# Kernel optimization log

Measured on AMD Instinct MI355X. Metric: run time of the kernel, lower is better.

Reference implementation:

```python
import jax, jax.numpy as jnp
import numpy as np
from jax import lax

HEADS, DIM_HEAD = 4, 64
INNER = HEADS * DIM_HEAD              # 256
FEAT_DIM = MAP_DIM = OUT_DIM = 128
EXPANDED = 4 * OUT_DIM                # 512 (MBConv expansion)
MAP_SIZE = (8, 8, 8)
EPS = 1e-5


def conv3d(x, w, groups=1):
    # x: NCDHW, w: OIDHW ([out, in/groups, kd, kh, kw]); stride 1, 'same' padding
    return lax.conv_general_dilated(x, w, (1, 1, 1), 'SAME',
                                    feature_group_count=groups,
                                    dimension_numbers=('NCDHW', 'OIDHW', 'NCDHW'))


def inorm(x):
    # InstanceNorm3d (affine=False): normalize over spatial dims per sample/channel
    m = x.mean((2, 3, 4), keepdims=True)
    v = ((x - m) ** 2).mean((2, 3, 4), keepdims=True)
    return (x - m) * lax.rsqrt(v + EPS)


def _split_heads(t, spatial):
    # 'b (dim_head heads) d h w -> b heads (d h w) dim_head'
    B = t.shape[0]
    N = spatial[0] * spatial[1] * spatial[2]
    return t.reshape(B, DIM_HEAD, HEADS, N).transpose(0, 2, 3, 1)


def _merge_heads(t, spatial):
    # 'b heads n dim_head -> b (dim_head heads) d h w'
    B = t.shape[0]
    return t.transpose(0, 3, 1, 2).reshape(B, DIM_HEAD * HEADS, *spatial)


def setup_inputs() -> dict:
    key = jax.random.key(0)
    ks = jax.random.split(key, 16)
    r = lambda k, s: jax.random.normal(k, s, jnp.float32) * 0.05
    return {
        'x': jax.random.normal(ks[0], (2, FEAT_DIM, 24, 24, 24), jnp.float32),
        'semantic_map': jax.random.normal(ks[1], (2, MAP_DIM) + MAP_SIZE, jnp.float32),
        'w_fqv_dw': r(ks[2], (FEAT_DIM, 1, 3, 3, 3)),
        'w_fqv_pw': r(ks[3], (2 * INNER, FEAT_DIM, 1, 1, 1)),
        'w_mqv':    r(ks[4], (2 * INNER, MAP_DIM, 1, 1, 1)),
        'w_fout_dw': r(ks[5], (INNER, 1, 3, 3, 3)),
        'w_fout_pw': r(ks[6], (OUT_DIM, INNER, 1, 1, 1)),
        'w_mout':   r(ks[7], (MAP_DIM, INNER, 1, 1, 1)),
        'w_exp':    r(ks[8], (EXPANDED, OUT_DIM, 1, 1, 1)),
        'w_dw':     r(ks[9], (EXPANDED, 1, 3, 3, 3)),
        'w_se1':    r(ks[10], (EXPANDED // 4, EXPANDED, 1, 1, 1)),
        'b_se1':    jnp.zeros((EXPANDED // 4,), jnp.float32),
        'w_se2':    r(ks[11], (EXPANDED, EXPANDED // 4, 1, 1, 1)),
        'b_se2':    jnp.zeros((EXPANDED,), jnp.float32),
        'w_pw':     r(ks[12], (OUT_DIM, EXPANDED, 1, 1, 1)),
    }


def _mbconv(x, w_exp, w_dw, w_se1, b_se1, w_se2, b_se2, w_pw):
    # MBConv (preact ConvNormAct blocks, InstanceNorm + ReLU, SE, identity shortcut)
    h = conv3d(jax.nn.relu(inorm(x)), w_exp)
    h = conv3d(jax.nn.relu(inorm(h)), w_dw, groups=EXPANDED)
    s = h.mean((2, 3, 4), keepdims=True)                       # squeeze
    s = jax.nn.relu(conv3d(s, w_se1) + b_se1[None, :, None, None, None])
    s = jax.nn.sigmoid(conv3d(s, w_se2) + b_se2[None, :, None, None, None])
    h = h * s
    h = conv3d(inorm(h), w_pw)                                 # pointwise, act=False
    return h + x


def reference(x, semantic_map, w_fqv_dw, w_fqv_pw, w_mqv, w_fout_dw, w_fout_pw,
              w_mout, w_exp, w_dw, w_se1, b_se1, w_se2, b_se2, w_pw):
    B, C, D, H, W = x.shape
    feat = inorm(x)
    m = inorm(semantic_map)

    # QV projections: depthwise-separable for feat, 1x1 for map
    fqv = conv3d(conv3d(feat, w_fqv_dw, groups=FEAT_DIM), w_fqv_pw)
    fq, fv = jnp.split(fqv, 2, axis=1)
    mqv = conv3d(m, w_mqv)
    mq, mv = jnp.split(mqv, 2, axis=1)

    fq = _split_heads(fq, (D, H, W))   # [B, h, Nf, dh]
    fv = _split_heads(fv, (D, H, W))
    mq = _split_heads(mq, MAP_SIZE)    # [B, h, Nm, dh]
    mv = _split_heads(mv, MAP_SIZE)

    # shared score matrix, dual-direction softmax
    attn = jnp.einsum('bhid,bhjd->bhij', fq, mq) * (DIM_HEAD ** -0.5)
    feat_map_attn = jax.nn.softmax(attn, axis=-1)   # over map tokens j
    map_feat_attn = jax.nn.softmax(attn, axis=-2)   # over feat tokens i

    feat_out = jnp.einsum('bhij,bhjd->bhid', feat_map_attn, mv)   # [B,h,Nf,dh]
    map_out = jnp.einsum('bhji,bhjd->bhid', map_feat_attn, fv)    # [B,h,Nm,dh]

    feat_out = _merge_heads(feat_out, (D, H, W))
    map_out = _merge_heads(map_out, MAP_SIZE)

    feat_out = conv3d(conv3d(feat_out, w_fout_dw, groups=INNER), w_fout_pw)
    map_out = conv3d(map_out, w_mout)

    out = feat_out + x   # shortcut is identity (feat_dim == out_dim)
    out = _mbconv(out, w_exp, w_dw, w_se1, b_se1, w_se2, b_se2, w_pw)
    map_out = map_out + semantic_map
    return out, map_out
```

## Files before the change

### kernel.cpp

```cpp
#include <hip/hip_runtime.h>
#include <hip/hip_bf16.h>
#include <cstddef>

#define NF 13824
#define NM 512
#define NIC 27

typedef __attribute__((ext_vector_type(8))) short bf16x8;
typedef __attribute__((ext_vector_type(4))) float f32x4;

__device__ __forceinline__ void gload16(const float* g, float* l){
  __builtin_amdgcn_global_load_lds((const __attribute__((address_space(1))) void*)g,
                                   (__attribute__((address_space(3))) void*)l, 16, 0, 0);
}

__global__ void k_transpose6(const float* __restrict__ s0, float* __restrict__ d0,
                             const float* __restrict__ s1, float* __restrict__ d1,
                             const float* __restrict__ s2, float* __restrict__ d2,
                             const float* __restrict__ s3, float* __restrict__ d3,
                             const float* __restrict__ s4, float* __restrict__ d4,
                             const float* __restrict__ s5, float* __restrict__ d5){
  const float* W; float* WT; int Cout, Cin;
  switch (blockIdx.y){
    case 0: W=s0; WT=d0; Cout=512; Cin=128; break;
    case 1: W=s1; WT=d1; Cout=512; Cin=128; break;
    case 2: W=s2; WT=d2; Cout=128; Cin=256; break;
    case 3: W=s3; WT=d3; Cout=128; Cin=256; break;
    case 4: W=s4; WT=d4; Cout=512; Cin=128; break;
    default: W=s5; WT=d5; Cout=128; Cin=512; break;
  }
  int idx = blockIdx.x*256 + threadIdx.x;
  if (idx >= Cout*Cin) return;
  int co = idx / Cin, ci = idx % Cin;
  WT[(size_t)ci*Cout + co] = W[idx];
}

__global__ void k_stats(const float* __restrict__ in, float2* __restrict__ st, int N,
                        float2* __restrict__ tf){
  int row = blockIdx.x;
  const float* p = in + (size_t)row*N;
  float s=0.f, q=0.f;
  int n4 = N/4;
  for (int i=threadIdx.x; i<n4; i+=256){
    float4 v = *(const float4*)(p + i*4);
    s += v.x+v.y+v.z+v.w;
    q += v.x*v.x+v.y*v.y+v.z*v.z+v.w*v.w;
  }
  __shared__ float rs[256], rq[256];
  rs[threadIdx.x]=s; rq[threadIdx.x]=q;
  __syncthreads();
  for (int o=128;o>0;o>>=1){
    if (threadIdx.x<o){ rs[threadIdx.x]+=rs[threadIdx.x+o]; rq[threadIdx.x]+=rq[threadIdx.x+o]; }
    __syncthreads();
  }
  if (threadIdx.x==0){
    float m = rs[0]/N;
    float v = rq[0]/N - m*m;
    if (v<0.f) v=0.f;
    st[row] = make_float2(m, v);
    if (tf){
      float a = rsqrtf(v + 1e-5f);
      tf[row] = make_float2(a, -m*a);
    }
  }
}

__global__ void k_make_tf(const float2* __restrict__ st, const float* __restrict__ sbuf,
                          float2* __restrict__ tf, int rows){
  int i = blockIdx.x*256 + threadIdx.x;
  if (i>=rows) return;
  float s = sbuf ? sbuf[i] : 1.f;
  float2 mv = st[i];
  float a = s*rsqrtf(s*s*mv.y + 1e-5f);
  tf[i] = make_float2(a, -mv.x*a);
}

__global__ void k_red(const float2* __restrict__ part, int nparts, int rows,
                      float invN, float2* __restrict__ tf){
  int w = threadIdx.x>>6, l = threadIdx.x&63;
  int row = blockIdx.x*4 + w;
  if (row >= rows) return;
  const float2* p = part + (size_t)row*nparts;
  float s=0.f, q=0.f;
  for (int k=l; k<nparts; k+=64){ float2 v = p[k]; s += v.x; q += v.y; }
  s += __shfl_xor(s,1); s += __shfl_xor(s,2); s += __shfl_xor(s,4);
  s += __shfl_xor(s,8); s += __shfl_xor(s,16); s += __shfl_xor(s,32);
  q += __shfl_xor(q,1); q += __shfl_xor(q,2); q += __shfl_xor(q,4);
  q += __shfl_xor(q,8); q += __shfl_xor(q,16); q += __shfl_xor(q,32);
  if (l==0){
    float m = s*invN;
    float v = q*invN - m*m;
    if (v<0.f) v=0.f;
    float a = rsqrtf(v + 1e-5f);
    tf[row] = make_float2(a, -m*a);
  }
}

__global__ void k_act(const float* __restrict__ in, const float2* __restrict__ tf,
                      float* __restrict__ outp){
  int i = blockIdx.x*256 + threadIdx.x;
  int n4 = i*4;
  int bc = n4 / NF;
  float2 t = tf[bc];
  float4 v = *(const float4*)(in + n4);
  v.x = fmaxf(t.x*v.x + t.y, 0.f);
  v.y = fmaxf(t.x*v.y + t.y, 0.f);
  v.z = fmaxf(t.x*v.z + t.y, 0.f);
  v.w = fmaxf(t.x*v.w + t.y, 0.f);
  *(float4*)(outp + n4) = v;
}

__global__ void k_fold(const float* __restrict__ wt, const float2* __restrict__ tf,
                       float* __restrict__ wf, float* __restrict__ bias){
  int co = blockIdx.x;
  int b  = blockIdx.y;
  float partb = 0.f;
  for (int ci=threadIdx.x; ci<512; ci+=256){
    float w = wt[ci*128 + co];
    float2 t = tf[b*512 + ci];
    wf[((size_t)b*512 + ci)*128 + co] = w * t.x;
    partb += w * t.y;
  }
  __shared__ float red[256];
  red[threadIdx.x] = partb; __syncthreads();
  for (int o=128;o>0;o>>=1){ if (threadIdx.x<o) red[threadIdx.x]+=red[threadIdx.x+o]; __syncthreads(); }
  if (threadIdx.x==0) bias[b*128 + co] = red[0];
}

__global__ __launch_bounds__(256) void k_dw3t(const float* __restrict__ in, const float* __restrict__ w,
                      const float2* __restrict__ tf, float* __restrict__ out,
                      int C, int relu, float2* __restrict__ stout){
  int bc = blockIdx.x;
  int c = bc % C;
  __shared__ float lds[4 + 26*728];
  __shared__ float rs2[256], rq2[256];
  float a = 1.f, bb = 0.f;
  if (tf){ float2 t = tf[bc]; a=t.x; bb=t.y; }

  {
    float4* l4 = (float4*)lds;
    float4 z = make_float4(0.f,0.f,0.f,0.f);
    for (int i=threadIdx.x; i<(4+26*728)/4; i+=256) l4[i] = z;
  }
  __syncthreads();

  const float* pin = in + (size_t)bc*NF;
  for (int i=threadIdx.x; i<NF/4; i+=256){
    int n = i*4;
    int d = n/576, r2 = n%576;
    int h = r2/24, wq = r2%24;
    float4 v = *(const float4*)(pin + n);
    float v0 = a*v.x+bb, v1 = a*v.y+bb, v2 = a*v.z+bb, v3 = a*v.w+bb;
    if (relu){ v0=fmaxf(v0,0.f); v1=fmaxf(v1,0.f); v2=fmaxf(v2,0.f); v3=fmaxf(v3,0.f); }
    *(float4*)(lds + 4 + (d+1)*728 + (h+1)*28 + wq) = make_float4(v0,v1,v2,v3);
  }

  const float* wc = w + c*27;
  float wr[27];
  #pragma unroll
  for (int k=0;k<27;k++) wr[k] = wc[k];
  __syncthreads();

  float ss=0.f, sq=0.f;
  for (int r = threadIdx.x; r < 576; r += 256){
    int d = r/24, h = r%24;
    float acc[24];
    #pragma unroll
    for (int i=0;i<24;i++) acc[i] = 0.f;
    #pragma unroll
    for (int kd=0;kd<3;kd++){
      #pragma unroll
      for (int kh=0;kh<3;kh++){
        const float* row = lds + 4 + (d+kd)*728 + (h+kh)*28;
        float rr[24];
        #pragma unroll
        for (int q=0;q<6;q++){
          float4 v4 = *(const float4*)(row + 4*q);
          rr[4*q]=v4.x; rr[4*q+1]=v4.y; rr[4*q+2]=v4.z; rr[4*q+3]=v4.w;
        }
        float rl = row[-1];
        float rrgt = row[24];
        float w0 = wr[kd*9+kh*3+0], w1 = wr[kd*9+kh*3+1], w2 = wr[kd*9+kh*3+2];
        acc[0] += w0*rl + w1*rr[0] + w2*rr[1];
        #pragma unroll
        for (int i=1;i<23;i++) acc[i] += w0*rr[i-1] + w1*rr[i] + w2*rr[i+1];
        acc[23] += w0*rr[22] + w1*rr[23] + w2*rrgt;
      }
    }
    if (stout){
      #pragma unroll
      for (int i=0;i<24;i++){ ss += acc[i]; sq += acc[i]*acc[i]; }
    }
    float* op = out + (size_t)bc*NF + r*24;
    #pragma unroll
    for (int q=0;q<6;q++)
      *(float4*)(op + 4*q) = make_float4(acc[4*q],acc[4*q+1],acc[4*q+2],acc[4*q+3]);
  }
  if (stout){
    rs2[threadIdx.x]=ss; rq2[threadIdx.x]=sq;
    __syncthreads();
    for (int o=128;o>0;o>>=1){
      if (threadIdx.x<o){ rs2[threadIdx.x]+=rs2[threadIdx.x+o]; rq2[threadIdx.x]+=rq2[threadIdx.x+o]; }
      __syncthreads();
    }
    if (threadIdx.x==0){
      float m = rs2[0]/NF;
      float v = rq2[0]/NF - m*m;
      stout[bc] = make_float2(m, v>0.f? v:0.f);
    }
  }
}

__global__ __launch_bounds__(256) void k_pw2(const float* __restrict__ in, const float* __restrict__ Wt,
                    const float* __restrict__ bias,
                    int Cin, int Cout, int N, int wstride,
                    const float* __restrict__ res,
                    float* __restrict__ out0,
                    __hip_bfloat16* __restrict__ qnm, __hip_bfloat16* __restrict__ vdm,
                    int mode, float2* __restrict__ part, int nparts){
  int b = blockIdx.z;
  int n0 = blockIdx.x*64, co0 = blockIdx.y*128;
  int t = threadIdx.x;
  int tx = t & 15, tyy = t >> 4;
  int wv = t >> 6, ln = t & 63;
  __shared__ float wl[2][32*128];
  __shared__ float il[2][32*64];
  float acc[8][4] = {};
  const float* inb = in + (size_t)b*Cin*N;
  const float* wb  = Wt + (size_t)b*wstride;

  int wrow = (ln>>5), wcol = (ln&31)*4;
  int irow = (ln>>4), icol = (ln&15)*4;

  auto STAGE = [&](int c0, int buf){
    #pragma unroll
    for (int k=0;k<4;k++){
      int row = wv*8 + 2*k + wrow;
      gload16(wb + (size_t)(c0+row)*Cout + co0 + wcol, &wl[buf][row*128 + wcol]);
    }
    #pragma unroll
    for (int k=0;k<2;k++){
      int row = wv*8 + 4*k + irow;
      gload16(inb + (size_t)(c0+row)*N + n0 + icol, &il[buf][row*64 + icol]);
    }
  };

  STAGE(0, 0);
  __syncthreads();

  int nc = Cin >> 5;
  int cur = 0;
  for (int c=0; c<nc; c++){
    if (c+1 < nc) STAGE((c+1)*32, cur^1);
    #pragma unroll
    for (int ci=0;ci<32;ci++){
      const float* wr2 = &wl[cur][ci*128 + tyy*8];
      float4 w0 = *(const float4*)(wr2);
      float4 w1 = *(const float4*)(wr2+4);
      float4 b4 = *(const float4*)&il[cur][ci*64 + tx*4];
      acc[0][0]+=w0.x*b4.x; acc[0][1]+=w0.x*b4.y; acc[0][2]+=w0.x*b4.z; acc[0][3]+=w0.x*b4.w;
      acc[1][0]+=w0.y*b4.x; acc[1][1]+=w0.y*b4.y; acc[1][2]+=w0.y*b4.z; acc[1][3]+=w0.y*b4.w;
      acc[2][0]+=w0.z*b4.x; acc[2][1]+=w0.z*b4.y; acc[2][2]+=w0.z*b4.z; acc[2][3]+=w0.z*b4.w;
      acc[3][0]+=w0.w*b4.x; acc[3][1]+=w0.w*b4.y; acc[3][2]+=w0.w*b4.z; acc[3][3]+=w0.w*b4.w;
      acc[4][0]+=w1.x*b4.x; acc[4][1]+=w1.x*b4.y; acc[4][2]+=w1.x*b4.z; acc[4][3]+=w1.x*b4.w;
      acc[5][0]+=w1.y*b4.x; acc[5][1]+=w1.y*b4.y; acc[5][2]+=w1.y*b4.z; acc[5][3]+=w1.y*b4.w;
      acc[6][0]+=w1.z*b4.x; acc[6][1]+=w1.z*b4.y; acc[6][2]+=w1.z*b4.z; acc[6][3]+=w1.z*b4.w;
      acc[7][0]+=w1.w*b4.x; acc[7][1]+=w1.w*b4.y; acc[7][2]+=w1.w*b4.z; acc[7][3]+=w1.w*b4.w;
    }
    __syncthreads();
    cur ^= 1;
  }

  if (mode==0){
    #pragma unroll
    for (int i=0;i<8;i++){
      int co = co0 + tyy*8 + i;
      float bco = bias ? bias[b*Cout + co] : 0.f;
      float* op = out0 + ((size_t)b*Cout + co)*N;
      float sv=0.f, qv=0.f;
      #pragma unroll
      for (int j=0;j<4;j++){
        int n = n0 + tx*4 + j;
        float v = acc[i][j] + bco;
        if (res) v += res[((size_t)b*Cout + co)*N + n];
        op[n] = v;
        sv += v; qv += v*v;
      }
      if (part){
        sv += __shfl_xor(sv,1); sv += __shfl_xor(sv,2); sv += __shfl_xor(sv,4); sv += __shfl_xor(sv,8);
        qv += __shfl_xor(qv,1); qv += __shfl_xor(qv,2); qv += __shfl_xor(qv,4); qv += __shfl_xor(qv,8);
        if (tx==0)
          part[(size_t)(b*Cout + co)*nparts + blockIdx.x] = make_float2(sv, qv);
      }
    }
  } else {
    bool isq = (co0 < 256);
    #pragma unroll
    for (int i=0;i<8;i++){
      int co = co0 + tyy*8 + i;
      int head = co & 3, dd = (co & 255) >> 2;
      int bhid = b*4 + head;
      #pragma unroll
      for (int j=0;j<4;j++){
        int n = n0 + tx*4 + j;
        __hip_bfloat16 v = __float2bfloat16(acc[i][j]);
        if (isq) qnm[((size_t)bhid*N + n)*64 + dd] = v;
        else     vdm[((size_t)(bhid*64 + dd))*N + n] = v;
      }
    }
  }
}

__global__ __launch_bounds__(256) void k_pw(const float* __restrict__ in, const float* __restrict__ WT,
                    const float2* __restrict__ tf, int relu,
                    int Cin, int Cout, int N,
                    const float* __restrict__ res,
                    float* __restrict__ out0,
                    __hip_bfloat16* __restrict__ qnm, __hip_bfloat16* __restrict__ vdm,
                    int mode){
  int b = blockIdx.z;
  int n0 = blockIdx.x*64, co0 = blockIdx.y*64;
  int tx = threadIdx.x & 15, ty = threadIdx.x >> 4;
  int cc = threadIdx.x & 63, g = threadIdx.x >> 6;
  __shared__ float wl[32][68];
  __shared__ float il[32][68];
  float acc[4][4] = {};
  const float* inb = in + (size_t)b*Cin*N;

  float rw[8], rv[8], ta[8], tb[8];
  #pragma unroll
  for (int rr=0;rr<8;rr++){ ta[rr]=1.f; tb[rr]=0.f; }
  #pragma unroll
  for (int rr=0;rr<8;rr++){
    int ci = g + 4*rr;
    rw[rr] = WT[(size_t)ci*Cout + co0 + cc];
    rv[rr] = inb[(size_t)ci*N + n0 + cc];
    if (tf){ float2 t = tf[b*Cin + ci]; ta[rr]=t.x; tb[rr]=t.y; }
  }

  for (int c0=0;c0<Cin;c0+=32){
    __syncthreads();
    #pragma unroll
    for (int rr=0;rr<8;rr++){
      int ci = g + 4*rr;
      wl[ci][cc] = rw[rr];
      float v = ta[rr]*rv[rr] + tb[rr];
      if (relu) v = fmaxf(v, 0.f);
      il[ci][cc] = v;
    }
    __syncthreads();
    if (c0+32 < Cin){
      int c0n = c0+32;
      #pragma unroll
      for (int rr=0;rr<8;rr++){
        int ci = g + 4*rr;
        rw[rr] = WT[(size_t)(c0n+ci)*Cout + co0 + cc];
        rv[rr] = inb[(size_t)(c0n+ci)*N + n0 + cc];
        if (tf){ float2 t = tf[b*Cin + c0n + ci]; ta[rr]=t.x; tb[rr]=t.y; }
      }
    }
    #pragma unroll
    for (int ci=0;ci<32;ci++){
      float4 a4 = *(const float4*)&wl[ci][ty*4];
      float4 b4 = *(const float4*)&il[ci][tx*4];
      acc[0][0]+=a4.x*b4.x; acc[0][1]+=a4.x*b4.y; acc[0][2]+=a4.x*b4.z; acc[0][3]+=a4.x*b4.w;
      acc[1][0]+=a4.y*b4.x; acc[1][1]+=a4.y*b4.y; acc[1][2]+=a4.y*b4.z; acc[1][3]+=a4.y*b4.w;
      acc[2][0]+=a4.z*b4.x; acc[2][1]+=a4.z*b4.y; acc[2][2]+=a4.z*b4.z; acc[2][3]+=a4.z*b4.w;
      acc[3][0]+=a4.w*b4.x; acc[3][1]+=a4.w*b4.y; acc[3][2]+=a4.w*b4.z; acc[3][3]+=a4.w*b4.w;
    }
  }
  if (mode==0){
    #pragma unroll
    for (int i=0;i<4;i++){
      int co = co0 + ty*4 + i;
      float* op = out0 + ((size_t)b*Cout + co)*N;
      #pragma unroll
      for (int j=0;j<4;j++){
        int n = n0 + tx*4 + j;
        float v = acc[i][j];
        if (res) v += res[((size_t)b*Cout + co)*N + n];
        op[n] = v;
      }
    }
  } else {
    int ccbase = (co0 & 255) + ty*4;
    int dd = ccbase >> 2;
    bool isq = (co0 < 256);
    #pragma unroll
    for (int i=0;i<4;i++){
      int bhid = b*4 + i;
      #pragma unroll
      for (int j=0;j<4;j++){
        int n = n0 + tx*4 + j;
        __hip_bfloat16 v = __float2bfloat16(acc[i][j]);
        if (isq) qnm[((size_t)bhid*N + n)*64 + dd] = v;
        else     vdm[((size_t)(bhid*64 + dd))*N + n] = v;
      }
    }
  }
}

__global__ __launch_bounds__(256) void k_attn(const __hip_bfloat16* __restrict__ qf,
    const __hip_bfloat16* __restrict__ qm, const __hip_bfloat16* __restrict__ vm,
    const __hip_bfloat16* __restrict__ vf,
    float* __restrict__ fo, float* __restrict__ num, float* __restrict__ cs){
  __shared__ __hip_bfloat16 pl[4][2][2][16][40];
  __shared__ float rsl[4][32];
  int bid = blockIdx.x;
  int sub = bid >> 1;
  int w = threadIdx.x>>6, l = threadIdx.x&63;
  int lr = l&15, lg = l>>4;

  if (bid & 1){
    int bh = sub/108, b = bh>>2, h = bh&3;
    int i0 = (sub%108)*128 + w*32;
    bf16x8 aq[2][2];
    #pragma unroll
    for (int g=0; g<2; g++){
      const __hip_bfloat16* qb = qf + ((size_t)bh*NF + i0 + g*16 + lr)*64 + lg*8;
      aq[g][0] = *(const bf16x8*)(qb);
      aq[g][1] = *(const bf16x8*)(qb + 32);
    }
    f32x4 facc[2][4];
    #pragma unroll
    for (int g=0; g<2; g++)
      #pragma unroll
      for (int t=0;t<4;t++){ facc[g][t][0]=0.f; facc[g][t][1]=0.f; facc[g][t][2]=0.f; facc[g][t][3]=0.f; }
    float rs[2][4] = {};
    const __hip_bfloat16* kbase = qm + ((size_t)bh*NM + lr)*64 + lg*8;
    const __hip_bfloat16* vbase = vm + ((size_t)bh*64 + lr)*NM + lg*8;

    auto fcomp = [&](bf16x8 K0, bf16x8 K1, bf16x8 K2, bf16x8 K3,
                     bf16x8 V0, bf16x8 V1, bf16x8 V2, bf16x8 V3, int SET){
      #pragma unroll
      for (int g=0; g<2; g++){
        f32x4 s0 = {0.f,0.f,0.f,0.f}, s1 = {0.f,0.f,0.f,0.f};
        s0 = __builtin_amdgcn_mfma_f32_16x16x32_bf16(aq[g][0], K0, s0, 0,0,0);
        s0 = __builtin_amdgcn_mfma_f32_16x16x32_bf16(aq[g][1], K1, s0, 0,0,0);
        s1 = __builtin_amdgcn_mfma_f32_16x16x32_bf16(aq[g][0], K2, s1, 0,0,0);
        s1 = __builtin_amdgcn_mfma_f32_16x16x32_bf16(aq[g][1], K3, s1, 0,0,0);
        #pragma unroll
        for (int r=0;r<4;r++){
          float p0 = __expf(s0[r]*0.125f);
          float p1 = __expf(s1[r]*0.125f);
          pl[w][SET][g][4*lg+r][lr]    = __float2bfloat16(p0);
          pl[w][SET][g][4*lg+r][16+lr] = __float2bfloat16(p1);
          rs[g][r] += p0 + p1;
        }
      }
      #pragma unroll
      for (int g=0; g<2; g++){
        bf16x8 bp = *(const bf16x8*)&pl[w][SET][g][lr][lg*8];
        facc[g][0] = __builtin_amdgcn_mfma_f32_16x16x32_bf16(V0, bp, facc[g][0], 0,0,0);
        facc[g][1] = __builtin_amdgcn_mfma_f32_16x16x32_bf16(V1, bp, facc[g][1], 0,0,0);
        facc[g][2] = __builtin_amdgcn_mfma_f32_16x16x32_bf16(V2, bp, facc[g][2], 0,0,0);
        facc[g][3] = __builtin_amdgcn_mfma_f32_16x16x32_bf16(V3, bp, facc[g][3], 0,0,0);
      }
    };

    bf16x8 kA0,kA1,kA2,kA3,vA0,vA1,vA2,vA3;
    bf16x8 kB0,kB1,kB2,kB3,vB0,vB1,vB2,vB3;
    #define FLOAD(KP,VP,J0) \
      KP##0 = *(const bf16x8*)(kbase + (size_t)(J0)*64); \
      KP##1 = *(const bf16x8*)(kbase + (size_t)(J0)*64 + 32); \
      KP##2 = *(const bf16x8*)(kbase + (size_t)(J0)*64 + 1024); \
      KP##3 = *(const bf16x8*)(kbase + (size_t)(J0)*64 + 1056); \
      VP##0 = *(const bf16x8*)(vbase + (J0)); \
      VP##1 = *(const bf16x8*)(vbase + 16*NM + (J0)); \
      VP##2 = *(const bf16x8*)(vbase + 32*NM + (J0)); \
      VP##3 = *(const bf16x8*)(vbase + 48*NM + (J0));

    FLOAD(kA,vA,0)
    for (int jt=0; jt<16; jt+=2){
      FLOAD(kB,vB,(jt+1)*32)
      fcomp(kA0,kA1,kA2,kA3,vA0,vA1,vA2,vA3,0);
      if (jt+2 < 16){ FLOAD(kA,vA,(jt+2)*32) }
      fcomp(kB0,kB1,kB2,kB3,vB0,vB1,vB2,vB3,1);
    }
    #undef FLOAD

    #pragma unroll
    for (int g=0; g<2; g++)
      #pragma unroll
      for (int r=0;r<4;r++){
        float v = rs[g][r];
        v += __shfl_xor(v,1); v += __shfl_xor(v,2); v += __shfl_xor(v,4); v += __shfl_xor(v,8);
        if (lr==0) rsl[w][g*16 + 4*lg+r] = v;
      }
    __syncthreads();
    #pragma unroll
    for (int g=0; g<2; g++){
      float inv = 1.f / rsl[w][g*16 + lr];
      #pragma unroll
      for (int dt=0; dt<4; dt++){
        #pragma unroll
        for (int r=0;r<4;r++){
          int d = dt*16 + 4*lg + r;
          fo[((size_t)(b*256 + d*4 + h))*NF + i0 + g*16 + lr] = facc[g][dt][r]*inv;
        }
      }
    }
  } else {
    int ic = sub%27, jb = (sub/27)&3, bh = sub/108;
    int jt0 = jb*128 + w*16;
    int jt1 = jt0 + 64;
    bf16x8 am[2][2];
    {
      const __hip_bfloat16* ab0 = qm + ((size_t)bh*NM + jt0 + lr)*64 + lg*8;
      const __hip_bfloat16* ab1 = qm + ((size_t)bh*NM + jt1 + lr)*64 + lg*8;
      am[0][0] = *(const bf16x8*)(ab0);
      am[0][1] = *(const bf16x8*)(ab0 + 32);
      am[1][0] = *(const bf16x8*)(ab1);
      am[1][1] = *(const bf16x8*)(ab1 + 32);
    }
    f32x4 macc[2][4];
    #pragma unroll
    for (int jg=0;jg<2;jg++)
      #pragma unroll
      for (int t=0;t<4;t++){ macc[jg][t][0]=0.f; macc[jg][t][1]=0.f; macc[jg][t][2]=0.f; macc[jg][t][3]=0.f; }
    float csr[2][4] = {};
    const __hip_bfloat16* fbase  = qf + ((size_t)bh*NF + lr)*64 + lg*8;
    const __hip_bfloat16* vfbase = vf + ((size_t)bh*64 + lr)*NF + lg*8;

    auto mcomp = [&](bf16x8 F0, bf16x8 F1, bf16x8 F2, bf16x8 F3,
                     bf16x8 V0, bf16x8 V1, bf16x8 V2, bf16x8 V3, int SET){
      #pragma unroll
      for (int jg=0;jg<2;jg++){
        f32x4 s0 = {0.f,0.f,0.f,0.f}, s1 = {0.f,0.f,0.f,0.f};
        s0 = __builtin_amdgcn_mfma_f32_16x16x32_bf16(am[jg][0], F0, s0, 0,0,0);
        s0 = __builtin_amdgcn_mfma_f32_16x16x32_bf16(am[jg][1], F1, s0, 0,0,0);
        s1 = __builtin_amdgcn_mfma_f32_16x16x32_bf16(am[jg][0], F2, s1, 0,0,0);
        s1 = __builtin_amdgcn_mfma_f32_16x16x32_bf16(am[jg][1], F3, s1, 0,0,0);
        #pragma unroll
        for (int r=0;r<4;r++){
          float p0 = __expf(s0[r]*0.125f);
          float p1 = __expf(s1[r]*0.125f);
          pl[w][SET][jg][4*lg+r][lr]    = __float2bfloat16(p0);
          pl[w][SET][jg][4*lg+r][16+lr] = __float2bfloat16(p1);
          csr[jg][r] += p0 + p1;
        }
      }
      #pragma unroll
      for (int jg=0;jg<2;jg++){
        bf16x8 bp = *(const bf16x8*)&pl[w][SET][jg][lr][lg*8];
        macc[jg][0] = __builtin_amdgcn_mfma_f32_16x16x32_bf16(V0, bp, macc[jg][0], 0,0,0);
        macc[jg][1] = __builtin_amdgcn_mfma_f32_16x16x32_bf16(V1, bp, macc[jg][1], 0,0,0);
        macc[jg][2] = __builtin_amdgcn_mfma_f32_16x16x32_bf16(V2, bp, macc[jg][2], 0,0,0);
        macc[jg][3] = __builtin_amdgcn_mfma_f32_16x16x32_bf16(V3, bp, macc[jg][3], 0,0,0);
      }
    };

    bf16x8 fA0,fA1,fA2,fA3,vA0,vA1,vA2,vA3;
    bf16x8 fB0,fB1,fB2,fB3,vB0,vB1,vB2,vB3;
    #define MLOAD(FP,VP,I0) \
      FP##0 = *(const bf16x8*)(fbase + (size_t)(I0)*64); \
      FP##1 = *(const bf16x8*)(fbase + (size_t)(I0)*64 + 32); \
      FP##2 = *(const bf16x8*)(fbase + (size_t)(I0)*64 + 1024); \
      FP##3 = *(const bf16x8*)(fbase + (size_t)(I0)*64 + 1056); \
      VP##0 = *(const bf16x8*)(vfbase + (size_t)(I0)); \
      VP##1 = *(const bf16x8*)(vfbase + (size_t)16*NF + (I0)); \
      VP##2 = *(const bf16x8*)(vfbase + (size_t)32*NF + (I0)); \
      VP##3 = *(const bf16x8*)(vfbase + (size_t)48*NF + (I0));

    int ibase = ic*512;
    MLOAD(fA,vA, ibase)
    for (int is=0; is<16; is+=2){
      MLOAD(fB,vB, ibase + (is+1)*32)
      mcomp(fA0,fA1,fA2,fA3,vA0,vA1,vA2,vA3,0);
      if (is+2<16){ MLOAD(fA,vA, ibase + (is+2)*32) }
      mcomp(fB0,fB1,fB2,fB3,vB0,vB1,vB2,vB3,1);
    }
    #undef MLOAD

    size_t nb = ((size_t)(ic*8 + bh)*64)*512;
    #pragma unroll
    for (int jg=0;jg<2;jg++){
      int jt = jg ? jt1 : jt0;
      #pragma unroll
      for (int dt=0;dt<4;dt++){
        #pragma unroll
        for (int r=0;r<4;r++){
          num[nb + (size_t)(dt*16 + 4*lg + r)*512 + jt + lr] = macc[jg][dt][r];
        }
      }
    }
    #pragma unroll
    for (int jg=0;jg<2;jg++){
      int jt = jg ? jt1 : jt0;
      #pragma unroll
      for (int r=0;r<4;r++){
        float v = csr[jg][r];
        v += __shfl_xor(v,1); v += __shfl_xor(v,2); v += __shfl_xor(v,4); v += __shfl_xor(v,8);
        if (lr==0) cs[(size_t)(ic*8 + bh)*512 + jt + 4*lg + r] = v;
      }
    }
  }
}

__global__ void k_comb(const float* __restrict__ num, const float* __restrict__ cs,
                       float* __restrict__ ma){
  int idx = blockIdx.x*256 + threadIdx.x;
  if (idx >= 8*512*64) return;
  int bh = idx>>15; int rem = idx&32767; int j = rem>>6; int d = rem&63;
  float s=0.f, c=0.f;
  for (int ic=0;ic<NIC;ic++){
    s += num[((size_t)(ic*8+bh)*64 + d)*512 + j];
    c += cs[(size_t)(ic*8+bh)*512 + j];
  }
  int b = bh>>2, h = bh&3;
  ma[((size_t)(b*256 + d*4 + h))*NM + j] = s/c;
}

__global__ void k_se(const float2* __restrict__ st, const float* __restrict__ w1, const float* __restrict__ b1,
                     const float* __restrict__ w2, const float* __restrict__ b2, float* __restrict__ sout){
  int b = blockIdx.x; int t = threadIdx.x;
  __shared__ float mean[512]; __shared__ float s1[128];
  mean[t]     = st[b*512 + t].x;
  mean[t+256] = st[b*512 + t + 256].x;
  __syncthreads();
  if (t<128){
    float a = b1[t];
    for (int c=0;c<512;c++) a += w1[t*512+c]*mean[c];
    s1[t] = fmaxf(a, 0.f);
  }
  __syncthreads();
  for (int o=t;o<512;o+=256){
    float a = b2[o];
    for (int c=0;c<128;c++) a += w2[o*128+c]*s1[c];
    sout[b*512+o] = 1.f/(1.f+__expf(-a));
  }
}

extern "C" void kernel_launch(void* const* d_in, const int* in_sizes, int n_in,
                              void* d_out, int out_size, void* d_ws, size_t ws_size,
                              hipStream_t stream){
  const float* x     = (const float*)d_in[0];
  const float* smap  = (const float*)d_in[1];
  const float* wfdw  = (const float*)d_in[2];
  const float* wfpw  = (const float*)d_in[3];
  const float* wmqv  = (const float*)d_in[4];
  const float* wodw  = (const float*)d_in[5];
  const float* wopw  = (const float*)d_in[6];
  const float* wmout = (const float*)d_in[7];
  const float* wexp  = (const float*)d_in[8];
  const float* wdw   = (const float*)d_in[9];
  const float* wse1  = (const float*)d_in[10];
  const float* bse1  = (const float*)d_in[11];
  const float* wse2  = (const float*)d_in[12];
  const float* bse2  = (const float*)d_in[13];
  const float* wpw   = (const float*)d_in[14];

  float* out  = (float*)d_out;
  float* mout = out + (size_t)2*128*NF;

  float* W = (float*)d_ws;
  size_t o = 0;
  __hip_bfloat16* qf = (__hip_bfloat16*)(W + o); o += (size_t)8*NF*32;
  __hip_bfloat16* vf = (__hip_bfloat16*)(W + o); o += (size_t)8*NF*32;
  float* fdw  = W + o; o += (size_t)2*128*NF;
  float* num  = W + o; o += (size_t)NIC*8*64*512;
  __hip_bfloat16* qm = (__hip_bfloat16*)(W + o); o += 8*NM*32;
  __hip_bfloat16* vm = (__hip_bfloat16*)(W + o); o += 8*NM*32;
  float* csb  = W + o; o += (size_t)NIC*8*512;
  float* ma   = W + o; o += (size_t)2*256*NM;
  float* h2   = (float*)d_ws;
  float* fo   = W + o; o += (size_t)2*256*NF;
  float* fdw2 = W + o; o += (size_t)2*256*NF;
  float* h1 = fo;
  float* wTf  = W + o; o += 512*128;
  float* wTm  = W + o; o += 512*128;
  float* wTo  = W + o; o += 128*256;
  float* wTmo = W + o; o += 128*256;
  float* wTe  = W + o; o += 512*128;
  float* wTp  = W + o; o += 128*512;
  float* wfP  = W + o; o += (size_t)2*512*128;
  float* biasP= W + o; o += 2*128;
  float2* partO = (float2*)(W+o); o += (size_t)2*256*216;
  float2* partH1= (float2*)(W+o); o += (size_t)2*1024*216;
  float2* tfO = (float2*)(W+o); o += 512;
  float2* tfH1= (float2*)(W+o); o += 2048;
  float2* stA = (float2*)(W+o); o += 512;
  float2* tfA = (float2*)(W+o); o += 512;
  float2* stM = (float2*)(W+o); o += 512;
  float2* tfM = (float2*)(W+o); o += 512;
  float2* stH2= (float2*)(W+o); o += 2048;
  float2* tfH = (float2*)(W+o); o += 2048;
  float* sbuf = W + o; o += 1024;
  (void)ws_size; (void)in_sizes; (void)n_in; (void)out_size;

  k_transpose6<<<dim3(256,6),256,0,stream>>>(wfpw,wTf, wmqv,wTm, wopw,wTo, wmout,wTmo, wexp,wTe, wpw,wTp);

  k_stats<<<256,256,0,stream>>>(x, stA, NF, tfA);
  k_dw3t<<<256,256,0,stream>>>(x, wfdw, tfA, fdw, 128, 0, nullptr);
  k_pw2<<<dim3(216,4,2),256,0,stream>>>(fdw, wTf, nullptr, 128,512,NF,0, nullptr, nullptr, qf, vf, 1, nullptr,0);

  k_stats<<<256,256,0,stream>>>(smap, stM, NM, tfM);
  k_pw<<<dim3(8,8,2),256,0,stream>>>(smap, wTm, tfM,0, 128,512,NM, nullptr, nullptr, qm, vm, 1);

  k_attn<<<dim3(1728),256,0,stream>>>(qf, qm, vm, vf, fo, num, csb);
  k_comb<<<1024,256,0,stream>>>(num, csb, ma);

  k_dw3t<<<512,256,0,stream>>>(fo, wodw, nullptr, fdw2, 256, 0, nullptr);
  k_pw2<<<dim3(216,1,2),256,0,stream>>>(fdw2, wTo, nullptr, 256,128,NF,0, x, out, nullptr,nullptr, 0, partO,216);
  k_pw<<<dim3(8,2,2),256,0,stream>>>(ma, wTmo, nullptr,0, 256,128,NM, smap, mout, nullptr,nullptr, 0);

  k_red<<<64,256,0,stream>>>(partO, 216, 256, 1.f/NF, tfO);
  k_act<<<3456,256,0,stream>>>(out, tfO, fdw);
  k_pw2<<<dim3(216,4,2),256,0,stream>>>(fdw, wTe, nullptr, 128,512,NF,0, nullptr, h1, nullptr,nullptr, 0, partH1,216);

  k_red<<<256,256,0,stream>>>(partH1, 216, 1024, 1.f/NF, tfH1);
  k_dw3t<<<1024,256,0,stream>>>(h1, wdw, tfH1, h2, 512, 1, stH2);

  k_se<<<2,256,0,stream>>>(stH2, wse1,bse1,wse2,bse2, sbuf);
  k_make_tf<<<4,256,0,stream>>>(stH2, sbuf, tfH, 1024);
  k_fold<<<dim3(128,2),256,0,stream>>>(wTp, tfH, wfP, biasP);
  k_pw2<<<dim3(216,1,2),256,0,stream>>>(h2, wfP, biasP, 512,128,NF,512*128, out, out, nullptr,nullptr, 0, nullptr,0);
}
```

Before: 570.4 us.

## Stage shared feature Q/V tiles in LDS for map-direction attention

In the map-token branch of the attention kernel, all four waves of a block previously loaded the same feature-query and feature-value tiles from global memory into registers on their own. They now load each 32-token tile cooperatively into double-buffered LDS with direct global-to-LDS loads, using XOR swizzling against bank conflicts, and each wave reads its MFMA operands from LDS. This is meant to cut redundant global/L2 traffic by sharing tiles across waves. It costs 16 KB of extra LDS and a block-wide barrier every iteration, which may reduce occupancy and add sync stalls.

```diff
diff --git a/kernel.cpp b/kernel.cpp
--- a/kernel.cpp
+++ b/kernel.cpp
@@ -406,6 +406,8 @@
     float* __restrict__ fo, float* __restrict__ num, float* __restrict__ cs){
   __shared__ __hip_bfloat16 pl[4][2][2][16][40];
   __shared__ float rsl[4][32];
+  __shared__ __hip_bfloat16 fstage[2][2048];
+  __shared__ __hip_bfloat16 vstage[2][2048];
   int bid = blockIdx.x;
   int sub = bid >> 1;
   int w = threadIdx.x>>6, l = threadIdx.x&63;
@@ -519,11 +521,35 @@
       #pragma unroll
       for (int t=0;t<4;t++){ macc[jg][t][0]=0.f; macc[jg][t][1]=0.f; macc[jg][t][2]=0.f; macc[jg][t][3]=0.f; }
     float csr[2][4] = {};
-    const __hip_bfloat16* fbase  = qf + ((size_t)bh*NF + lr)*64 + lg*8;
-    const __hip_bfloat16* vfbase = vf + ((size_t)bh*64 + lr)*NF + lg*8;
-
-    auto mcomp = [&](bf16x8 F0, bf16x8 F1, bf16x8 F2, bf16x8 F3,
-                     bf16x8 V0, bf16x8 V1, bf16x8 V2, bf16x8 V3, int SET){
+    const __hip_bfloat16* qfb = qf + (size_t)bh*NF*64;
+    const __hip_bfloat16* vfb = vf + (size_t)bh*64*NF;
+
+    int t64 = w*64 + l;
+    int fp = t64*16;
+    int fq = fp ^ (((fp>>7)&7)<<4);
+    int vp = t64*16;
+    int vq = vp ^ (((vp>>6)&3)<<4);
+    int vrow = vq >> 6;
+    int vcol = (vq & 63) >> 1;
+
+    auto STAGE = [&](int i0t, int buf){
+      gload16((const float*)(qfb + (size_t)i0t*64 + (fq>>1)), (float*)&fstage[buf][w*512]);
+      gload16((const float*)(vfb + (size_t)vrow*NF + i0t + vcol), (float*)&vstage[buf][w*512]);
+    };
+    auto ldF = [&](int buf, int row, int seg)->bf16x8 {
+      int byte = row*128 + ((seg ^ (row&7))<<4);
+      return *(const bf16x8*)((const char*)&fstage[buf][0] + byte);
+    };
+    auto ldV = [&](int buf, int row, int seg)->bf16x8 {
+      int byte = row*64 + ((seg ^ (row&3))<<4);
+      return *(const bf16x8*)((const char*)&vstage[buf][0] + byte);
+    };
+
+    auto mcomp = [&](int buf, int SET){
+      bf16x8 F0 = ldF(buf, lr,    lg);
+      bf16x8 F1 = ldF(buf, lr,    lg+4);
+      bf16x8 F2 = ldF(buf, 16+lr, lg);
+      bf16x8 F3 = ldF(buf, 16+lr, lg+4);
       #pragma unroll
       for (int jg=0;jg<2;jg++){
         f32x4 s0 = {0.f,0.f,0.f,0.f}, s1 = {0.f,0.f,0.f,0.f};
@@ -540,6 +566,10 @@
           csr[jg][r] += p0 + p1;
         }
       }
+      bf16x8 V0 = ldV(buf, lr,    lg);
+      bf16x8 V1 = ldV(buf, 16+lr, lg);
+      bf16x8 V2 = ldV(buf, 32+lr, lg);
+      bf16x8 V3 = ldV(buf, 48+lr, lg);
       #pragma unroll
       for (int jg=0;jg<2;jg++){
         bf16x8 bp = *(const bf16x8*)&pl[w][SET][jg][lr][lg*8];
@@ -550,27 +580,14 @@
       }
     };
 
-    bf16x8 fA0,fA1,fA2,fA3,vA0,vA1,vA2,vA3;
-    bf16x8 fB0,fB1,fB2,fB3,vB0,vB1,vB2,vB3;
-    #define MLOAD(FP,VP,I0) \
-      FP##0 = *(const bf16x8*)(fbase + (size_t)(I0)*64); \
-      FP##1 = *(const bf16x8*)(fbase + (size_t)(I0)*64 + 32); \
-      FP##2 = *(const bf16x8*)(fbase + (size_t)(I0)*64 + 1024); \
-      FP##3 = *(const bf16x8*)(fbase + (size_t)(I0)*64 + 1056); \
-      VP##0 = *(const bf16x8*)(vfbase + (size_t)(I0)); \
-      VP##1 = *(const bf16x8*)(vfbase + (size_t)16*NF + (I0)); \
-      VP##2 = *(const bf16x8*)(vfbase + (size_t)32*NF + (I0)); \
-      VP##3 = *(const bf16x8*)(vfbase + (size_t)48*NF + (I0));
-
     int ibase = ic*512;
-    MLOAD(fA,vA, ibase)
-    for (int is=0; is<16; is+=2){
-      MLOAD(fB,vB, ibase + (is+1)*32)
-      mcomp(fA0,fA1,fA2,fA3,vA0,vA1,vA2,vA3,0);
-      if (is+2<16){ MLOAD(fA,vA, ibase + (is+2)*32) }
-      mcomp(fB0,fB1,fB2,fB3,vB0,vB1,vB2,vB3,1);
-    }
-    #undef MLOAD
+    STAGE(ibase, 0);
+    __syncthreads();
+    for (int is=0; is<16; is++){
+      if (is+1 < 16) STAGE(ibase + (is+1)*32, (is&1)^1);
+      mcomp(is&1, is&1);
+      __syncthreads();
+    }
 
     size_t nb = ((size_t)(ic*8 + bh)*64)*512;
     #pragma unroll
```

Measured after the change: 571.1 us. No clear change (+0.1%).
